# Performance work log

Measured on AMD Instinct MI355X. Metric: run time of the kernel, lower is better.

## Reference

```python
import jax, jax.numpy as jnp
import numpy as np

CL = 256   # context_length (global in original code)
IL = 64    # inst_length (global in original code)
PC, CH1, CH2, CH3 = 64, 128, 256, 256
CK1, CK2, CK3 = 3, 3, 3
CS1, CS2, CS3 = 1, 2, 2
CP1, CP2, CP3 = 1, 1, 1
BCH1, BCH2, BCH3 = 64, 128, 256
F1, OUT = 1024, 2
B = 2048
C3_OUT = 64 * CH3            # 16384, per __init__ formula with CL-1=255
F1_IN = C3_OUT + BCH3        # 16640


def _conv1d(x, W, b, stride, pad):
    # x: [B, Cin, L], W: [Cout, Cin, K]
    y = jax.lax.conv_general_dilated(x, W, window_strides=(stride,),
                                     padding=[(pad, pad)],
                                     dimension_numbers=("NCH", "OIH", "NCH"))
    return y + b[None, :, None]


def setup_inputs() -> dict:
    key = jax.random.key(0)
    ks = jax.random.split(key, 20)
    s = lambda *sh: 1.0 / np.sqrt(np.prod(sh[1:]))
    def w(k, *sh):
        return jax.random.normal(k, sh, dtype=jnp.float32) * s(*sh)
    return {
        "x": jax.random.normal(ks[0], (B, CL * IL), dtype=jnp.float32),
        "Wp": w(ks[1], PC, IL, 2), "bp": jnp.zeros((PC,), jnp.float32),
        "W1": w(ks[2], CH1, PC, CK1), "b1": jnp.zeros((CH1,), jnp.float32),
        "W2": w(ks[3], CH2, CH1, CK2), "b2": jnp.zeros((CH2,), jnp.float32),
        "W3": w(ks[4], CH3, CH2, CK3), "b3": jnp.zeros((CH3,), jnp.float32),
        "Wb1": w(ks[5], BCH1, IL), "bb1": jnp.zeros((BCH1,), jnp.float32),
        "Wb2": w(ks[6], BCH2, BCH1), "bb2": jnp.zeros((BCH2,), jnp.float32),
        "Wb3": w(ks[7], BCH3, BCH2), "bb3": jnp.zeros((BCH3,), jnp.float32),
        "Wfc1": w(ks[8], F1, F1_IN), "bfc1": jnp.zeros((F1,), jnp.float32),
        "Wfc2": w(ks[9], OUT, F1), "bfc2": jnp.zeros((OUT,), jnp.float32),
    }


def reference(x, Wp, bp, W1, b1, W2, b2, W3, b3,
              Wb1, bb1, Wb2, bb2, Wb3, bb3, Wfc1, bfc1, Wfc2, bfc2):
    xr = x.reshape(-1, CL, IL).transpose(0, 2, 1)   # [B, IL, CL]
    x0 = xr[:, :, 0]                                 # [B, IL]
    # Fused replacement for the convp loop: kernel-2 conv over (x0, x_i)
    # y[:, :, i-1] = Wp[:,:,0] @ x0 + Wp[:,:,1] @ x_i + bp
    y = (jnp.einsum("bi,pi->bp", x0, Wp[:, :, 0])[:, :, None]
         + jnp.einsum("bic,pi->bpc", xr[:, :, 1:], Wp[:, :, 1])
         + bp[None, :, None])                        # [B, PC, CL-1]
    # bypass path on the first instruction (kernel-size-1 convs == matmuls)
    f = jax.nn.relu(x0 @ Wb1.T + bb1)
    f = jax.nn.relu(f @ Wb2.T + bb2)
    f = jax.nn.relu(f @ Wb3.T + bb3)                 # [B, BCH3]
    h = jax.nn.relu(y)
    h = jax.nn.relu(_conv1d(h, W1, b1, CS1, CP1))
    h = jax.nn.relu(_conv1d(h, W2, b2, CS2, CP2))
    h = jax.nn.relu(_conv1d(h, W3, b3, CS3, CP3))    # [B, CH3, 64]
    h = h.reshape(h.shape[0], C3_OUT)
    z = jnp.concatenate([h, f], axis=1)              # [B, F1_IN]
    z = jax.nn.relu(z @ Wfc1.T + bfc1)
    return z @ Wfc2.T + bfc2                         # [B, OUT]
```

## Files before the change

### kernel.cpp

```cpp
#include <hip/hip_runtime.h>
#include <cstdint>
#include <cstddef>

typedef __attribute__((ext_vector_type(8))) short bf16x8;
typedef __attribute__((ext_vector_type(8))) unsigned short ushort8;
typedef __attribute__((ext_vector_type(4))) float f32x4;

__device__ __forceinline__ unsigned short f2bf(float f){
  unsigned int u = __float_as_uint(f);
  unsigned int lsb = (u >> 16) & 1u;
  u += 0x7fffu + lsb;
  return (unsigned short)(u >> 16);
}

__device__ __forceinline__ void gload16(const void* g, void* l){
  __builtin_amdgcn_global_load_lds(
      (const __attribute__((address_space(1))) unsigned int*)g,
      (__attribute__((address_space(3))) unsigned int*)l, 16, 0, 0);
}

__global__ __launch_bounds__(256) void pack_w_bf16_kernel(const float* __restrict__ W,
    unsigned short* __restrict__ Wb, int COUT, int CIN){
  int idx = blockIdx.x*256 + threadIdx.x;
  int tot = COUT*CIN*3;
  if (idx >= tot) return;
  int o = idx/(CIN*3); int r = idx - o*(CIN*3); int kk = r/CIN; int ci = r - kk*CIN;
  Wb[idx] = f2bf(W[(o*CIN + ci)*3 + kk]);
}

__global__ __launch_bounds__(256) void pack_wp_kernel(const float* __restrict__ Wp,
                                                      unsigned short* __restrict__ Bw){
  int idx = blockIdx.x*256 + threadIdx.x;
  if (idx >= 64*128) return;
  int p = idx >> 7, k = idx & 127;
  float v = (k < 64) ? Wp[p*128 + k*2] : Wp[p*128 + (k-64)*2 + 1];
  Bw[idx] = f2bf(v);
}

__global__ __launch_bounds__(256) void f2bf_kernel(const float* __restrict__ src,
                                                   unsigned short* __restrict__ dst, int n){
  int i = blockIdx.x*256 + threadIdx.x;
  if (i < n) dst[i] = f2bf(src[i]);
}

__global__ __launch_bounds__(256) void zero_guards_kernel(unsigned short* __restrict__ buf,
                                                          int LINP, int CIN, int nb){
  int idx = blockIdx.x*256 + threadIdx.x;
  int per = 2*CIN/8;
  if (idx >= nb*per) return;
  int b = idx / per, r = idx - b*per;
  int g = r / (CIN/8), c8 = r - g*(CIN/8);
  ushort8 z = {0,0,0,0,0,0,0,0};
  *(ushort8*)(buf + ((size_t)b*LINP + (size_t)g*(LINP-1))*CIN + c8*8) = z;
}

__global__ __launch_bounds__(256) void branch_kernel(const float* __restrict__ x,
    const float* __restrict__ Wb1, const float* __restrict__ bb1,
    const float* __restrict__ Wb2, const float* __restrict__ bb2,
    const float* __restrict__ Wb3, const float* __restrict__ bb3,
    unsigned short* __restrict__ Hcat){
  __shared__ float s0[64], s1[64], s2[128];
  const int b = blockIdx.x, tid = threadIdx.x;
  const float* xb = x + (size_t)b*16384;
  if (tid < 64) s0[tid] = xb[tid];
  __syncthreads();
  if (tid < 64){
    float a = bb1[tid];
    for (int k=0;k<64;k++) a = fmaf(Wb1[tid*64+k], s0[k], a);
    s1[tid] = fmaxf(a, 0.f);
  }
  __syncthreads();
  if (tid < 128){
    float a = bb2[tid];
    for (int k=0;k<64;k++) a = fmaf(Wb2[tid*64+k], s1[k], a);
    s2[tid] = fmaxf(a, 0.f);
  }
  __syncthreads();
  float a = bb3[tid];
  for (int k=0;k<128;k++) a = fmaf(Wb3[tid*128+k], s2[k], a);
  Hcat[(size_t)b*16640 + 16384 + tid] = f2bf(fmaxf(a, 0.f));
}

__global__ __launch_bounds__(256) void h0_gemm_kernel(const float* __restrict__ x,
    const unsigned short* __restrict__ Bw, const float* __restrict__ bp,
    unsigned short* __restrict__ h0o){
  __shared__ __align__(16) char sAraw[128*256];
  __shared__ __align__(16) char sBraw[64*256];
  const int tid = threadIdx.x;
  const int m0 = blockIdx.x*128;
  #pragma unroll
  for (int i=0;i<16;i++){
    int j = tid + 256*i;
    int row = j >> 5, q = j & 31;
    int m = m0 + row;
    int b = m / 255, c = m - b*255;
    const float* xb = x + (size_t)b*16384;
    int k = q*4;
    const float* src = (k < 64) ? (xb + k) : (xb + (c+1)*64 + (k-64));
    float4 v = *(const float4*)src;
    ushort4 u; u.x=f2bf(v.x); u.y=f2bf(v.y); u.z=f2bf(v.z); u.w=f2bf(v.w);
    *(ushort4*)(sAraw + row*256 + ((k*2) ^ ((row&7)<<4))) = u;
  }
  #pragma unroll
  for (int i=0;i<4;i++){
    int j = tid + 256*i;
    int row = j >> 4, q = j & 15;
    int k = q*8;
    ushort8 u = *(const ushort8*)(Bw + row*128 + k);
    *(ushort8*)(sBraw + row*256 + ((k*2) ^ ((row&7)<<4))) = u;
  }
  __syncthreads();
  const int lane = tid & 63, wid = tid >> 6;
  const int lr = lane & 15, lg = lane >> 4;
  f32x4 acc[2][4];
  #pragma unroll
  for (int a=0;a<2;a++)
    #pragma unroll
    for (int j=0;j<4;j++) acc[a][j] = (f32x4){0,0,0,0};
  #pragma unroll
  for (int ks=0; ks<4; ks++){
    int k = ks*32 + lg*8;
    bf16x8 af[2], bfr[4];
    #pragma unroll
    for (int f=0; f<2; f++){
      int row = wid*32 + f*16 + lr;
      af[f] = *(const bf16x8*)(sAraw + row*256 + ((k*2) ^ ((row&7)<<4)));
    }
    #pragma unroll
    for (int f=0; f<4; f++){
      int row = f*16 + lr;
      bfr[f] = *(const bf16x8*)(sBraw + row*256 + ((k*2) ^ ((row&7)<<4)));
    }
    #pragma unroll
    for (int fi=0; fi<2; fi++)
      #pragma unroll
      for (int fj=0; fj<4; fj++)
        acc[fi][fj] = __builtin_amdgcn_mfma_f32_16x16x32_bf16(af[fi], bfr[fj], acc[fi][fj], 0,0,0);
  }
  #pragma unroll
  for (int fi=0; fi<2; fi++)
    #pragma unroll
    for (int fj=0; fj<4; fj++)
      #pragma unroll
      for (int j=0;j<4;j++){
        int m = m0 + wid*32 + fi*16 + lg*4 + j;
        int n = fj*16 + lr;
        int b = m / 255, t = m - b*255;
        h0o[((size_t)b*257 + t + 1)*64 + n] = f2bf(fmaxf(acc[fi][fj][j] + bp[n], 0.f));
      }
}

template<int CIN,int COUT,int S,int LINP,int LOUT,bool TO_HCAT>
__global__ __launch_bounds__(256) void conv_gemm_kernel(
    const unsigned short* __restrict__ in, const unsigned short* __restrict__ Wb,
    const float* __restrict__ bias, unsigned short* __restrict__ out){
  constexpr int K = 3*CIN;
  constexpr int KS = K/64;
  __shared__ __align__(16) char sA[2*128*128];
  __shared__ __align__(16) char sB[2*128*128];
  const int tid = threadIdx.x;
  int m0;
  {
    int bid = blockIdx.x, nwg = gridDim.x;
    if ((nwg & 7) == 0){ int q = nwg >> 3; m0 = ((bid & 7)*q + (bid >> 3))*128; }
    else m0 = bid*128;
  }
  const int n0 = blockIdx.y*128;
  const int lane = tid & 63, wid = tid >> 6;
  const int wm = wid >> 1, wn = wid & 1;
  const int lr = lane & 15, lg = lane >> 4;
  const int srow = lane >> 3;
  const int soff = (((lane&7) ^ srow) << 3);
  const unsigned short* abase[4];
  const unsigned short* bbase[4];
  #pragma unroll
  for (int s=0;s<4;s++){
    int row = wid*32 + s*8 + srow;
    int m = m0 + row;
    int b = m / LOUT, t = m - b*LOUT;
    abase[s] = in + ((size_t)b*LINP + (size_t)t*S)*CIN + soff;
    bbase[s] = Wb + (size_t)(n0+row)*K + soff;
  }
  f32x4 acc[4][4];
  #pragma unroll
  for (int i=0;i<4;i++)
    #pragma unroll
    for (int j=0;j<4;j++) acc[i][j] = (f32x4){0,0,0,0};

  auto stage = [&](int ks, int bufi){
    const int k0 = ks*64;
    #pragma unroll
    for (int s=0;s<4;s++){
      gload16(abase[s] + k0, sA + bufi*16384 + wid*4096 + s*1024);
      gload16(bbase[s] + k0, sB + bufi*16384 + wid*4096 + s*1024);
    }
  };
  stage(0, 0);
  __syncthreads();
  int buf = 0;
  #pragma unroll
  for (int ks=0; ks<KS; ks++){
    if (ks+1 < KS) stage(ks+1, buf^1);
    #pragma unroll
    for (int kss=0; kss<2; kss++){
      const int k = kss*32 + lg*8;
      bf16x8 af[4], bfr[4];
      #pragma unroll
      for (int f=0;f<4;f++){
        int ra = wm*64 + f*16 + lr;
        af[f]  = *(const bf16x8*)(sA + buf*16384 + ra*128 + ((k*2) ^ ((ra&7)<<4)));
        int rb = wn*64 + f*16 + lr;
        bfr[f] = *(const bf16x8*)(sB + buf*16384 + rb*128 + ((k*2) ^ ((rb&7)<<4)));
      }
      #pragma unroll
      for (int fi=0;fi<4;fi++)
        #pragma unroll
        for (int fj=0;fj<4;fj++)
          acc[fi][fj] = __builtin_amdgcn_mfma_f32_16x16x32_bf16(af[fi], bfr[fj], acc[fi][fj], 0,0,0);
    }
    __syncthreads();
    buf ^= 1;
  }
  #pragma unroll
  for (int fi=0;fi<4;fi++)
    #pragma unroll
    for (int fj=0;fj<4;fj++)
      #pragma unroll
      for (int j=0;j<4;j++){
        int m = m0 + wm*64 + fi*16 + lg*4 + j;
        int n = n0 + wn*64 + fj*16 + lr;
        int b = m / LOUT, t = m - b*LOUT;
        float val = fmaxf(acc[fi][fj][j] + bias[n], 0.f);
        if (TO_HCAT) out[(size_t)b*16640 + (size_t)n*64 + t] = f2bf(val);
        else         out[((size_t)b*(LOUT+2) + t + 1)*COUT + n] = f2bf(val);
      }
}

__global__ __launch_bounds__(256) void fc1_gemm_kernel(
    const unsigned short* __restrict__ A, const unsigned short* __restrict__ Bw,
    float* __restrict__ zp, int zoffm, int MT, int KZ){
  __shared__ __align__(16) char sA[2*128*128];
  __shared__ __align__(16) char sB[2*128*128];
  const int tid = threadIdx.x;
  const int nwg = gridDim.x;
  const int lgid = (blockIdx.x % 8)*(nwg/8) + blockIdx.x/8;
  const int kz  = lgid / (8*MT);
  const int rem = lgid % (8*MT);
  const int nt  = rem / MT;
  const int mt  = rem % MT;
  const int n0 = nt*128, m0 = mt*128;
  const int lane = tid & 63, wid = tid >> 6;
  const int wm = wid >> 1, wn = wid & 1;
  const int lr = lane & 15, lg = lane >> 4;
  const int srow = lane >> 3;
  const int soff = (((lane&7) ^ srow) << 3);
  f32x4 acc[4][4];
  #pragma unroll
  for (int i=0;i<4;i++)
    #pragma unroll
    for (int j=0;j<4;j++) acc[i][j] = (f32x4){0,0,0,0};
  const int it0 = (kz*260)/KZ, it1 = ((kz+1)*260)/KZ;

  auto stage = [&](int it, int bufi){
    const size_t k0 = (size_t)it*64;
    #pragma unroll
    for (int s=0;s<4;s++){
      int row = wid*32 + s*8 + srow;
      gload16(A  + (size_t)(m0+row)*16640 + k0 + soff, sA + bufi*16384 + wid*4096 + s*1024);
      gload16(Bw + (size_t)(n0+row)*16640 + k0 + soff, sB + bufi*16384 + wid*4096 + s*1024);
    }
  };
  stage(it0, 0);
  __syncthreads();
  int buf = 0;
  for (int it=it0; it<it1; ++it){
    if (it+1 < it1) stage(it+1, buf^1);
    #pragma unroll
    for (int ks=0; ks<2; ks++){
      const int k = ks*32 + lg*8;
      bf16x8 af[4], bfr[4];
      #pragma unroll
      for (int f=0;f<4;f++){
        int rowa = wm*64 + f*16 + lr;
        af[f]  = *(const bf16x8*)(sA + buf*16384 + rowa*128 + ((k*2) ^ ((rowa&7)<<4)));
        int rowb = wn*64 + f*16 + lr;
        bfr[f] = *(const bf16x8*)(sB + buf*16384 + rowb*128 + ((k*2) ^ ((rowb&7)<<4)));
      }
      #pragma unroll
      for (int fi=0;fi<4;fi++)
        #pragma unroll
        for (int fj=0;fj<4;fj++)
          acc[fi][fj] = __builtin_amdgcn_mfma_f32_16x16x32_bf16(af[fi], bfr[fj], acc[fi][fj], 0,0,0);
    }
    __syncthreads();
    buf ^= 1;
  }
  float* zo = zp + (size_t)kz*zoffm;
  #pragma unroll
  for (int fi=0;fi<4;fi++)
    #pragma unroll
    for (int fj=0;fj<4;fj++)
      #pragma unroll
      for (int j=0;j<4;j++){
        int m = m0 + wm*64 + fi*16 + lg*4 + j;
        int n = n0 + wn*64 + fj*16 + lr;
        zo[(size_t)m*1024 + n] = acc[fi][fj][j];
      }
}

__global__ __launch_bounds__(256) void fc2_kernel(const float* __restrict__ zp, int zoffm, int KZ,
    const float* __restrict__ bfc1, const float* __restrict__ Wfc2,
    const float* __restrict__ bfc2, float* __restrict__ out){
  __shared__ float red[4][2];
  const int b = blockIdx.x, tid = threadIdx.x;
  float a0 = 0.f, a1 = 0.f;
  for (int n = tid; n < 1024; n += 256){
    float s = bfc1[n];
    const float* zb = zp + (size_t)b*1024 + n;
    for (int kz = 0; kz < KZ; kz++) s += zb[(size_t)kz*zoffm];
    s = fmaxf(s, 0.f);
    a0 = fmaf(s, Wfc2[n], a0);
    a1 = fmaf(s, Wfc2[1024+n], a1);
  }
  #pragma unroll
  for (int m=32; m>=1; m>>=1){ a0 += __shfl_xor(a0, m, 64); a1 += __shfl_xor(a1, m, 64); }
  const int w = tid >> 6;
  if ((tid & 63) == 0){ red[w][0] = a0; red[w][1] = a1; }
  __syncthreads();
  if (tid == 0){
    out[(size_t)b*2]   = red[0][0]+red[1][0]+red[2][0]+red[3][0] + bfc2[0];
    out[(size_t)b*2+1] = red[0][1]+red[1][1]+red[2][1]+red[3][1] + bfc2[1];
  }
}

extern "C" void kernel_launch(void* const* d_in, const int* in_sizes, int n_in,
                              void* d_out, int out_size, void* d_ws, size_t ws_size,
                              hipStream_t stream){
  const float* x    = (const float*)d_in[0];
  const float* Wp   = (const float*)d_in[1];
  const float* bp   = (const float*)d_in[2];
  const float* W1   = (const float*)d_in[3];
  const float* b1   = (const float*)d_in[4];
  const float* W2   = (const float*)d_in[5];
  const float* b2   = (const float*)d_in[6];
  const float* W3   = (const float*)d_in[7];
  const float* b3   = (const float*)d_in[8];
  const float* Wb1  = (const float*)d_in[9];
  const float* bb1  = (const float*)d_in[10];
  const float* Wb2  = (const float*)d_in[11];
  const float* bb2  = (const float*)d_in[12];
  const float* Wb3  = (const float*)d_in[13];
  const float* bb3  = (const float*)d_in[14];
  const float* Wfc1 = (const float*)d_in[15];
  const float* bfc1 = (const float*)d_in[16];
  const float* Wfc2 = (const float*)d_in[17];
  const float* bfc2 = (const float*)d_in[18];
  float* out = (float*)d_out;

  size_t off = 0;
  char* basep = (char*)d_ws;
  auto carve = [&](size_t bytes)->char*{
    char* q = basep + off; off += (bytes + 255) & ~(size_t)255; return q;
  };
  unsigned short* W1b   = (unsigned short*)carve((size_t)128*3*64*2);
  unsigned short* W2b   = (unsigned short*)carve((size_t)256*3*128*2);
  unsigned short* W3b   = (unsigned short*)carve((size_t)256*3*256*2);
  unsigned short* Bwp   = (unsigned short*)carve((size_t)64*128*2);
  unsigned short* Wfc1b = (unsigned short*)carve((size_t)1024*16640*2);
  size_t fixed = off;

  int Bc = 128, KZ = 64;
  {
    const int bcs[5] = {2048, 1024, 512, 256, 128};
    const int kzs[5] = {4, 8, 16, 32, 64};
    for (int i = 0; i < 5; i++){
      size_t b = bcs[i];
      size_t need = fixed + b*((size_t)66560+65792+33280) + (size_t)kzs[i]*b*4096 + 16*256;
      if (need <= ws_size){ Bc = bcs[i]; KZ = kzs[i]; break; }
    }
  }
  const int NC = 2048/Bc;
  const int MT = Bc/128;
  unsigned short* buf1 = (unsigned short*)carve((size_t)Bc*66560);
  unsigned short* buf2 = (unsigned short*)carve((size_t)Bc*65792);
  unsigned short* Hcat = (unsigned short*)carve((size_t)Bc*33280);
  float*          zp   = (float*)carve((size_t)KZ*Bc*4096);
  const int zoffm = Bc*1024;

  hipLaunchKernelGGL(pack_w_bf16_kernel, dim3((128*64*3+255)/256), dim3(256), 0, stream, W1, W1b, 128, 64);
  hipLaunchKernelGGL(pack_w_bf16_kernel, dim3((256*128*3+255)/256), dim3(256), 0, stream, W2, W2b, 256, 128);
  hipLaunchKernelGGL(pack_w_bf16_kernel, dim3((256*256*3+255)/256), dim3(256), 0, stream, W3, W3b, 256, 256);
  hipLaunchKernelGGL(pack_wp_kernel, dim3(32), dim3(256), 0, stream, Wp, Bwp);
  hipLaunchKernelGGL(f2bf_kernel, dim3((17039360+255)/256), dim3(256), 0, stream, Wfc1, Wfc1b, 17039360);

  for (int c = 0; c < NC; ++c){
    const float* xc = x + (size_t)c*Bc*16384;
    hipLaunchKernelGGL(zero_guards_kernel, dim3((Bc*2*64/8+255)/256), dim3(256), 0, stream,
                       buf1, 257, 64, Bc);
    hipLaunchKernelGGL(zero_guards_kernel, dim3((Bc*2*128/8+255)/256), dim3(256), 0, stream,
                       buf2, 257, 128, Bc);
    hipLaunchKernelGGL(branch_kernel, dim3(Bc), dim3(256), 0, stream,
                       xc, Wb1, bb1, Wb2, bb2, Wb3, bb3, Hcat);
    hipLaunchKernelGGL(h0_gemm_kernel, dim3(Bc*255/128), dim3(256), 0, stream, xc, Bwp, bp, buf1);
    hipLaunchKernelGGL((conv_gemm_kernel<64,128,1,257,255,false>), dim3(Bc*255/128, 1), dim3(256), 0, stream,
                       buf1, W1b, b1, buf2);
    hipLaunchKernelGGL(zero_guards_kernel, dim3((Bc*2*256/8+255)/256), dim3(256), 0, stream,
                       buf1, 130, 256, Bc);
    hipLaunchKernelGGL((conv_gemm_kernel<128,256,2,257,128,false>), dim3(Bc, 2), dim3(256), 0, stream,
                       buf2, W2b, b2, buf1);
    hipLaunchKernelGGL((conv_gemm_kernel<256,256,2,130,64,true>), dim3(Bc/2, 2), dim3(256), 0, stream,
                       buf1, W3b, b3, Hcat);
    hipLaunchKernelGGL(fc1_gemm_kernel, dim3(8*MT*KZ), dim3(256), 0, stream,
                       Hcat, Wfc1b, zp, zoffm, MT, KZ);
    hipLaunchKernelGGL(fc2_kernel, dim3(Bc), dim3(256), 0, stream,
                       zp, zoffm, KZ, bfc1, Wfc2, bfc2, out + (size_t)c*Bc*2);
  }
}
```

Before: 547.5 us.

## Replace im2col conv GEMM with per-batch input window staged once in LDS

```diff
diff --git a/kernel.cpp b/kernel.cpp
--- a/kernel.cpp
+++ b/kernel.cpp
@@ -150,70 +150,82 @@
       }
 }
 
-template<int CIN,int COUT,int S,int LINP,int LOUT,bool TO_HCAT>
-__global__ __launch_bounds__(256) void conv_gemm_kernel(
+template<int CIN,int COUT,int S,int LOUT,int PADIN,int PADOUT,int BM,bool TO_HCAT>
+__global__ __launch_bounds__(256) void conv_win_kernel(
     const unsigned short* __restrict__ in, const unsigned short* __restrict__ Wb,
     const float* __restrict__ bias, unsigned short* __restrict__ out){
-  constexpr int K = 3*CIN;
-  constexpr int KS = K/64;
-  __shared__ __align__(16) char sA[2*128*128];
-  __shared__ __align__(16) char sB[2*128*128];
-  const int tid = threadIdx.x;
-  int m0;
-  {
-    int bid = blockIdx.x, nwg = gridDim.x;
-    if ((nwg & 7) == 0){ int q = nwg >> 3; m0 = ((bid & 7)*q + (bid >> 3))*128; }
-    else m0 = bid*128;
-  }
-  const int n0 = blockIdx.y*128;
-  const int lane = tid & 63, wid = tid >> 6;
+  constexpr int K3  = 3*CIN, NCH = K3/64;
+  constexpr int MPB = (LOUT + BM - 1)/BM;
+  constexpr int NT  = COUT/128;
+  constexpr int MF  = BM/32;
+  constexpr int WR  = (BM-1)*S + 3;
+  constexpr int CP8 = CIN/8;
+  constexpr int CB  = CIN*2;
+  constexpr int NSLOT = WR*CP8;
+  __shared__ __align__(16) char SA[WR*CB];
+  __shared__ __align__(16) char SB[2*16384];
+  const int tid = threadIdx.x, lane = tid & 63, wid = tid >> 6;
+  int lgid;
+  { int bid = blockIdx.x, nwg = gridDim.x;
+    lgid = ((nwg & 7)==0) ? ((bid & 7)*(nwg>>3) + (bid>>3)) : bid; }
+  const int nt = lgid % NT;
+  const int tile = lgid / NT;
+  const int b = tile / MPB, mt = tile % MPB;
+  const int t0 = mt*BM, n0 = nt*128;
+  const unsigned short* Abase = in + ((size_t)b*PADIN + (size_t)t0*S)*CIN;
+  const int rowlim = PADIN - t0*S;
+
+  for (int i=0; i*256 < NSLOT; ++i){
+    int slot = i*256 + tid;
+    if (slot < NSLOT){
+      int row = slot/CP8, p = slot - row*CP8;
+      if (row < rowlim)
+        gload16(Abase + (size_t)row*CIN + ((p ^ ((row>>(S-1))&7))<<3), SA + slot*16);
+      else
+        *(ushort8*)(SA + slot*16) = (ushort8){0,0,0,0,0,0,0,0};
+    }
+  }
+  const int srow = lane >> 3;
+  const int bsoff = (((lane&7) ^ srow) << 3);
+  auto stageB = [&](int c, int bufi){
+    #pragma unroll
+    for (int s=0;s<4;s++){
+      int row = wid*32 + s*8 + srow;
+      gload16(Wb + (size_t)(n0+row)*K3 + c*64 + bsoff, SB + bufi*16384 + wid*4096 + s*1024);
+    }
+  };
+  stageB(0, 0);
+  __syncthreads();
+
   const int wm = wid >> 1, wn = wid & 1;
   const int lr = lane & 15, lg = lane >> 4;
-  const int srow = lane >> 3;
-  const int soff = (((lane&7) ^ srow) << 3);
-  const unsigned short* abase[4];
-  const unsigned short* bbase[4];
-  #pragma unroll
-  for (int s=0;s<4;s++){
-    int row = wid*32 + s*8 + srow;
-    int m = m0 + row;
-    int b = m / LOUT, t = m - b*LOUT;
-    abase[s] = in + ((size_t)b*LINP + (size_t)t*S)*CIN + soff;
-    bbase[s] = Wb + (size_t)(n0+row)*K + soff;
-  }
-  f32x4 acc[4][4];
-  #pragma unroll
-  for (int i=0;i<4;i++)
+  f32x4 acc[MF][4];
+  #pragma unroll
+  for (int i=0;i<MF;i++)
     #pragma unroll
     for (int j=0;j<4;j++) acc[i][j] = (f32x4){0,0,0,0};
 
-  auto stage = [&](int ks, int bufi){
-    const int k0 = ks*64;
-    #pragma unroll
-    for (int s=0;s<4;s++){
-      gload16(abase[s] + k0, sA + bufi*16384 + wid*4096 + s*1024);
-      gload16(bbase[s] + k0, sB + bufi*16384 + wid*4096 + s*1024);
-    }
-  };
-  stage(0, 0);
-  __syncthreads();
   int buf = 0;
   #pragma unroll
-  for (int ks=0; ks<KS; ks++){
-    if (ks+1 < KS) stage(ks+1, buf^1);
-    #pragma unroll
-    for (int kss=0; kss<2; kss++){
-      const int k = kss*32 + lg*8;
-      bf16x8 af[4], bfr[4];
+  for (int c=0;c<NCH;c++){
+    if (c+1 < NCH) stageB(c+1, buf^1);
+    const int kk = c/(CIN/64), cc = c - kk*(CIN/64);
+    #pragma unroll
+    for (int ks=0; ks<2; ks++){
+      bf16x8 af[MF], bfr[4];
+      #pragma unroll
+      for (int f=0;f<MF;f++){
+        int row = (wm*(MF*16) + f*16 + lr)*S + kk;
+        int ci = cc*8 + ks*4 + lg;
+        af[f] = *(const bf16x8*)(SA + (size_t)row*CB + ((ci ^ ((row>>(S-1))&7))<<4));
+      }
       #pragma unroll
       for (int f=0;f<4;f++){
-        int ra = wm*64 + f*16 + lr;
-        af[f]  = *(const bf16x8*)(sA + buf*16384 + ra*128 + ((k*2) ^ ((ra&7)<<4)));
         int rb = wn*64 + f*16 + lr;
-        bfr[f] = *(const bf16x8*)(sB + buf*16384 + rb*128 + ((k*2) ^ ((rb&7)<<4)));
-      }
-      #pragma unroll
-      for (int fi=0;fi<4;fi++)
+        bfr[f] = *(const bf16x8*)(SB + buf*16384 + rb*128 + (((ks*4+lg) ^ (rb&7))<<4));
+      }
+      #pragma unroll
+      for (int fi=0;fi<MF;fi++)
         #pragma unroll
         for (int fj=0;fj<4;fj++)
           acc[fi][fj] = __builtin_amdgcn_mfma_f32_16x16x32_bf16(af[fi], bfr[fj], acc[fi][fj], 0,0,0);
@@ -221,18 +233,20 @@
     __syncthreads();
     buf ^= 1;
   }
-  #pragma unroll
-  for (int fi=0;fi<4;fi++)
+
+  #pragma unroll
+  for (int fi=0;fi<MF;fi++)
     #pragma unroll
     for (int fj=0;fj<4;fj++)
       #pragma unroll
       for (int j=0;j<4;j++){
-        int m = m0 + wm*64 + fi*16 + lg*4 + j;
+        int t = t0 + wm*(MF*16) + fi*16 + lg*4 + j;
         int n = n0 + wn*64 + fj*16 + lr;
-        int b = m / LOUT, t = m - b*LOUT;
-        float val = fmaxf(acc[fi][fj][j] + bias[n], 0.f);
-        if (TO_HCAT) out[(size_t)b*16640 + (size_t)n*64 + t] = f2bf(val);
-        else         out[((size_t)b*(LOUT+2) + t + 1)*COUT + n] = f2bf(val);
+        if (MPB*BM == LOUT || t < LOUT){
+          float v = fmaxf(acc[fi][fj][j] + bias[n], 0.f);
+          if (TO_HCAT) out[(size_t)b*16640 + (size_t)n*64 + t] = f2bf(v);
+          else         out[((size_t)b*PADOUT + t + 1)*COUT + n] = f2bf(v);
+        }
       }
 }
 
@@ -402,14 +416,14 @@
     hipLaunchKernelGGL(branch_kernel, dim3(Bc), dim3(256), 0, stream,
                        xc, Wb1, bb1, Wb2, bb2, Wb3, bb3, Hcat);
     hipLaunchKernelGGL(h0_gemm_kernel, dim3(Bc*255/128), dim3(256), 0, stream, xc, Bwp, bp, buf1);
-    hipLaunchKernelGGL((conv_gemm_kernel<64,128,1,257,255,false>), dim3(Bc*255/128, 1), dim3(256), 0, stream,
-                       buf1, W1b, b1, buf2);
+    hipLaunchKernelGGL((conv_win_kernel<64,128,1,255,257,257,128,false>),
+                       dim3(Bc*2), dim3(256), 0, stream, buf1, W1b, b1, buf2);
     hipLaunchKernelGGL(zero_guards_kernel, dim3((Bc*2*256/8+255)/256), dim3(256), 0, stream,
                        buf1, 130, 256, Bc);
-    hipLaunchKernelGGL((conv_gemm_kernel<128,256,2,257,128,false>), dim3(Bc, 2), dim3(256), 0, stream,
-                       buf2, W2b, b2, buf1);
-    hipLaunchKernelGGL((conv_gemm_kernel<256,256,2,130,64,true>), dim3(Bc/2, 2), dim3(256), 0, stream,
-                       buf1, W3b, b3, Hcat);
+    hipLaunchKernelGGL((conv_win_kernel<128,256,2,128,257,130,64,false>),
+                       dim3(Bc*4), dim3(256), 0, stream, buf2, W2b, b2, buf1);
+    hipLaunchKernelGGL((conv_win_kernel<256,256,2,64,130,0,32,true>),
+                       dim3(Bc*4), dim3(256), 0, stream, buf1, W3b, b3, Hcat);
     hipLaunchKernelGGL(fc1_gemm_kernel, dim3(8*MT*KZ), dim3(256), 0, stream,
                        Hcat, Wfc1b, zp, zoffm, MT, KZ);
     hipLaunchKernelGGL(fc2_kernel, dim3(Bc), dim3(256), 0, stream,
```

Result: slower. 579.4 us (+5.8%).

## Use 256x128 single-buffered tiles with 512 threads in conv GEMMs

Applied to the files above, without the earlier changes.

```diff
diff --git a/kernel.cpp b/kernel.cpp
--- a/kernel.cpp
+++ b/kernel.cpp
@@ -151,19 +151,19 @@
 }
 
 template<int CIN,int COUT,int S,int LINP,int LOUT,bool TO_HCAT>
-__global__ __launch_bounds__(256) void conv_gemm_kernel(
+__global__ __launch_bounds__(512) void conv_gemm_kernel(
     const unsigned short* __restrict__ in, const unsigned short* __restrict__ Wb,
-    const float* __restrict__ bias, unsigned short* __restrict__ out){
+    const float* __restrict__ bias, unsigned short* __restrict__ out, int M){
   constexpr int K = 3*CIN;
   constexpr int KS = K/64;
-  __shared__ __align__(16) char sA[2*128*128];
-  __shared__ __align__(16) char sB[2*128*128];
+  __shared__ __align__(16) char sA[256*128];
+  __shared__ __align__(16) char sB[128*128];
   const int tid = threadIdx.x;
   int m0;
   {
     int bid = blockIdx.x, nwg = gridDim.x;
-    if ((nwg & 7) == 0){ int q = nwg >> 3; m0 = ((bid & 7)*q + (bid >> 3))*128; }
-    else m0 = bid*128;
+    if ((nwg & 7) == 0){ int q = nwg >> 3; m0 = ((bid & 7)*q + (bid >> 3))*256; }
+    else m0 = bid*256;
   }
   const int n0 = blockIdx.y*128;
   const int lane = tid & 63, wid = tid >> 6;
@@ -172,13 +172,17 @@
   const int srow = lane >> 3;
   const int soff = (((lane&7) ^ srow) << 3);
   const unsigned short* abase[4];
-  const unsigned short* bbase[4];
+  const unsigned short* bbase[2];
   #pragma unroll
   for (int s=0;s<4;s++){
-    int row = wid*32 + s*8 + srow;
-    int m = m0 + row;
+    int m = m0 + wid*32 + s*8 + srow;
+    if (m >= M) m = M-1;
     int b = m / LOUT, t = m - b*LOUT;
     abase[s] = in + ((size_t)b*LINP + (size_t)t*S)*CIN + soff;
+  }
+  #pragma unroll
+  for (int s=0;s<2;s++){
+    int row = wid*16 + s*8 + srow;
     bbase[s] = Wb + (size_t)(n0+row)*K + soff;
   }
   f32x4 acc[4][4];
@@ -187,20 +191,15 @@
     #pragma unroll
     for (int j=0;j<4;j++) acc[i][j] = (f32x4){0,0,0,0};
 
-  auto stage = [&](int ks, int bufi){
+  #pragma unroll
+  for (int ks=0; ks<KS; ks++){
     const int k0 = ks*64;
-    #pragma unroll
-    for (int s=0;s<4;s++){
-      gload16(abase[s] + k0, sA + bufi*16384 + wid*4096 + s*1024);
-      gload16(bbase[s] + k0, sB + bufi*16384 + wid*4096 + s*1024);
-    }
-  };
-  stage(0, 0);
-  __syncthreads();
-  int buf = 0;
-  #pragma unroll
-  for (int ks=0; ks<KS; ks++){
-    if (ks+1 < KS) stage(ks+1, buf^1);
+    __syncthreads();
+    #pragma unroll
+    for (int s=0;s<4;s++) gload16(abase[s] + k0, sA + wid*4096 + s*1024);
+    #pragma unroll
+    for (int s=0;s<2;s++) gload16(bbase[s] + k0, sB + wid*2048 + s*1024);
+    __syncthreads();
     #pragma unroll
     for (int kss=0; kss<2; kss++){
       const int k = kss*32 + lg*8;
@@ -208,9 +207,9 @@
       #pragma unroll
       for (int f=0;f<4;f++){
         int ra = wm*64 + f*16 + lr;
-        af[f]  = *(const bf16x8*)(sA + buf*16384 + ra*128 + ((k*2) ^ ((ra&7)<<4)));
+        af[f]  = *(const bf16x8*)(sA + ra*128 + ((k*2) ^ ((ra&7)<<4)));
         int rb = wn*64 + f*16 + lr;
-        bfr[f] = *(const bf16x8*)(sB + buf*16384 + rb*128 + ((k*2) ^ ((rb&7)<<4)));
+        bfr[f] = *(const bf16x8*)(sB + rb*128 + ((k*2) ^ ((rb&7)<<4)));
       }
       #pragma unroll
       for (int fi=0;fi<4;fi++)
@@ -218,8 +217,6 @@
         for (int fj=0;fj<4;fj++)
           acc[fi][fj] = __builtin_amdgcn_mfma_f32_16x16x32_bf16(af[fi], bfr[fj], acc[fi][fj], 0,0,0);
     }
-    __syncthreads();
-    buf ^= 1;
   }
   #pragma unroll
   for (int fi=0;fi<4;fi++)
@@ -229,10 +226,12 @@
       for (int j=0;j<4;j++){
         int m = m0 + wm*64 + fi*16 + lg*4 + j;
         int n = n0 + wn*64 + fj*16 + lr;
-        int b = m / LOUT, t = m - b*LOUT;
-        float val = fmaxf(acc[fi][fj][j] + bias[n], 0.f);
-        if (TO_HCAT) out[(size_t)b*16640 + (size_t)n*64 + t] = f2bf(val);
-        else         out[((size_t)b*(LOUT+2) + t + 1)*COUT + n] = f2bf(val);
+        if (m < M){
+          int b = m / LOUT, t = m - b*LOUT;
+          float val = fmaxf(acc[fi][fj][j] + bias[n], 0.f);
+          if (TO_HCAT) out[(size_t)b*16640 + (size_t)n*64 + t] = f2bf(val);
+          else         out[((size_t)b*(LOUT+2) + t + 1)*COUT + n] = f2bf(val);
+        }
       }
 }
 
@@ -402,14 +401,23 @@
     hipLaunchKernelGGL(branch_kernel, dim3(Bc), dim3(256), 0, stream,
                        xc, Wb1, bb1, Wb2, bb2, Wb3, bb3, Hcat);
     hipLaunchKernelGGL(h0_gemm_kernel, dim3(Bc*255/128), dim3(256), 0, stream, xc, Bwp, bp, buf1);
-    hipLaunchKernelGGL((conv_gemm_kernel<64,128,1,257,255,false>), dim3(Bc*255/128, 1), dim3(256), 0, stream,
-                       buf1, W1b, b1, buf2);
+    {
+      int M = Bc*255, gx = (M + 255)/256;
+      hipLaunchKernelGGL((conv_gemm_kernel<64,128,1,257,255,false>), dim3(gx, 1), dim3(512), 0, stream,
+                         buf1, W1b, b1, buf2, M);
+    }
     hipLaunchKernelGGL(zero_guards_kernel, dim3((Bc*2*256/8+255)/256), dim3(256), 0, stream,
                        buf1, 130, 256, Bc);
-    hipLaunchKernelGGL((conv_gemm_kernel<128,256,2,257,128,false>), dim3(Bc, 2), dim3(256), 0, stream,
-                       buf2, W2b, b2, buf1);
-    hipLaunchKernelGGL((conv_gemm_kernel<256,256,2,130,64,true>), dim3(Bc/2, 2), dim3(256), 0, stream,
-                       buf1, W3b, b3, Hcat);
+    {
+      int M = Bc*128;
+      hipLaunchKernelGGL((conv_gemm_kernel<128,256,2,257,128,false>), dim3(M/256, 2), dim3(512), 0, stream,
+                         buf2, W2b, b2, buf1, M);
+    }
+    {
+      int M = Bc*64;
+      hipLaunchKernelGGL((conv_gemm_kernel<256,256,2,130,64,true>), dim3(M/256, 2), dim3(512), 0, stream,
+                         buf1, W3b, b3, Hcat, M);
+    }
     hipLaunchKernelGGL(fc1_gemm_kernel, dim3(8*MT*KZ), dim3(256), 0, stream,
                        Hcat, Wfc1b, zp, zoffm, MT, KZ);
     hipLaunchKernelGGL(fc2_kernel, dim3(Bc), dim3(256), 0, stream,
```

Result: slower. 563.2 us (+2.9%).

## Fuse input projection and first conv into one per-sample kernel

Applied to the files above, without the earlier changes.

```diff
diff --git a/kernel.cpp b/kernel.cpp
--- a/kernel.cpp
+++ b/kernel.cpp
@@ -11,6 +11,11 @@
   unsigned int lsb = (u >> 16) & 1u;
   u += 0x7fffu + lsb;
   return (unsigned short)(u >> 16);
+}
+
+__device__ __forceinline__ ushort8 cvt8(const float4 a, const float4 b){
+  ushort8 u; u[0]=f2bf(a.x); u[1]=f2bf(a.y); u[2]=f2bf(a.z); u[3]=f2bf(a.w);
+  u[4]=f2bf(b.x); u[5]=f2bf(b.y); u[6]=f2bf(b.z); u[7]=f2bf(b.w); return u;
 }
 
 __device__ __forceinline__ void gload16(const void* g, void* l){
@@ -28,13 +33,12 @@
   Wb[idx] = f2bf(W[(o*CIN + ci)*3 + kk]);
 }
 
-__global__ __launch_bounds__(256) void pack_wp_kernel(const float* __restrict__ Wp,
-                                                      unsigned short* __restrict__ Bw){
+__global__ __launch_bounds__(256) void pack_bh_kernel(const float* __restrict__ Wp,
+                                                      unsigned short* __restrict__ Bh){
   int idx = blockIdx.x*256 + threadIdx.x;
-  if (idx >= 64*128) return;
-  int p = idx >> 7, k = idx & 127;
-  float v = (k < 64) ? Wp[p*128 + k*2] : Wp[p*128 + (k-64)*2 + 1];
-  Bw[idx] = f2bf(v);
+  if (idx >= 64*64) return;
+  int p = idx >> 6, i = idx & 63;
+  Bh[idx] = f2bf(Wp[p*128 + i*2 + 1]);
 }
 
 __global__ __launch_bounds__(256) void f2bf_kernel(const float* __restrict__ src,
@@ -81,73 +85,132 @@
   Hcat[(size_t)b*16640 + 16384 + tid] = f2bf(fmaxf(a, 0.f));
 }
 
-__global__ __launch_bounds__(256) void h0_gemm_kernel(const float* __restrict__ x,
-    const unsigned short* __restrict__ Bw, const float* __restrict__ bp,
-    unsigned short* __restrict__ h0o){
-  __shared__ __align__(16) char sAraw[128*256];
-  __shared__ __align__(16) char sBraw[64*256];
-  const int tid = threadIdx.x;
-  const int m0 = blockIdx.x*128;
-  #pragma unroll
-  for (int i=0;i<16;i++){
-    int j = tid + 256*i;
-    int row = j >> 5, q = j & 31;
-    int m = m0 + row;
-    int b = m / 255, c = m - b*255;
-    const float* xb = x + (size_t)b*16384;
-    int k = q*4;
-    const float* src = (k < 64) ? (xb + k) : (xb + (c+1)*64 + (k-64));
-    float4 v = *(const float4*)src;
-    ushort4 u; u.x=f2bf(v.x); u.y=f2bf(v.y); u.z=f2bf(v.z); u.w=f2bf(v.w);
-    *(ushort4*)(sAraw + row*256 + ((k*2) ^ ((row&7)<<4))) = u;
-  }
+__global__ __launch_bounds__(512) void fused1_kernel(
+    const float* __restrict__ x, const float* __restrict__ Wp, const float* __restrict__ bp,
+    const unsigned short* __restrict__ Bh, const unsigned short* __restrict__ W1b,
+    const float* __restrict__ b1, unsigned short* __restrict__ c1p){
+  __shared__ __align__(16) char S[115392];
+  constexpr int SX = 0;
+  constexpr int SH = 37008;
+  constexpr int SB = 74160;
+  constexpr int SW = 106928;
+  constexpr int SY = 115120;
+  const int b = blockIdx.x, tid = threadIdx.x;
+  const int lane = tid & 63, wv = tid >> 6;
+  const int lr = lane & 15, lg = lane >> 4;
+  const float* xg = x + (size_t)b*16384;
+
   #pragma unroll
   for (int i=0;i<4;i++){
-    int j = tid + 256*i;
-    int row = j >> 4, q = j & 15;
-    int k = q*8;
-    ushort8 u = *(const ushort8*)(Bw + row*128 + k);
-    *(ushort8*)(sBraw + row*256 + ((k*2) ^ ((row&7)<<4))) = u;
-  }
-  __syncthreads();
-  const int lane = tid & 63, wid = tid >> 6;
-  const int lr = lane & 15, lg = lane >> 4;
-  f32x4 acc[2][4];
-  #pragma unroll
-  for (int a=0;a<2;a++)
-    #pragma unroll
-    for (int j=0;j<4;j++) acc[a][j] = (f32x4){0,0,0,0};
-  #pragma unroll
-  for (int ks=0; ks<4; ks++){
-    int k = ks*32 + lg*8;
-    bf16x8 af[2], bfr[4];
-    #pragma unroll
-    for (int f=0; f<2; f++){
-      int row = wid*32 + f*16 + lr;
-      af[f] = *(const bf16x8*)(sAraw + row*256 + ((k*2) ^ ((row&7)<<4)));
-    }
-    #pragma unroll
-    for (int f=0; f<4; f++){
-      int row = f*16 + lr;
-      bfr[f] = *(const bf16x8*)(sBraw + row*256 + ((k*2) ^ ((row&7)<<4)));
-    }
-    #pragma unroll
-    for (int fi=0; fi<2; fi++)
-      #pragma unroll
-      for (int fj=0; fj<4; fj++)
-        acc[fi][fj] = __builtin_amdgcn_mfma_f32_16x16x32_bf16(af[fi], bfr[fj], acc[fi][fj], 0,0,0);
-  }
-  #pragma unroll
-  for (int fi=0; fi<2; fi++)
-    #pragma unroll
-    for (int fj=0; fj<4; fj++)
-      #pragma unroll
-      for (int j=0;j<4;j++){
-        int m = m0 + wid*32 + fi*16 + lg*4 + j;
-        int n = fj*16 + lr;
-        int b = m / 255, t = m - b*255;
-        h0o[((size_t)b*257 + t + 1)*64 + n] = f2bf(fmaxf(acc[fi][fj][j] + bp[n], 0.f));
-      }
+    int s = tid + 512*i;
+    int row = s>>3, sl = s&7;
+    const float4* src = (const float4*)(xg + row*64 + sl*8);
+    *(ushort8*)(S + SX + row*144 + sl*16) = cvt8(src[0], src[1]);
+  }
+  { int row = tid>>3, sl = tid&7;
+    ushort8 u = *(const ushort8*)(Bh + row*64 + sl*8);
+    *(ushort8*)(S + SW + row*128 + ((sl*16)^((row&7)<<4))) = u; }
+  ushort8 z8 = {0,0,0,0,0,0,0,0};
+  if (tid < 9)        *(ushort8*)(S + SX + 256*144 + tid*16) = z8;
+  else if (tid < 18)  *(ushort8*)(S + SH + 0*144   + (tid-9)*16) = z8;
+  else if (tid < 27)  *(ushort8*)(S + SH + 257*144 + (tid-18)*16) = z8;
+  if (tid < 64){
+    float a = bp[tid];
+    const float* wr = Wp + tid*128;
+    #pragma unroll 8
+    for (int i=0;i<64;i++) a = fmaf(wr[2*i], xg[i], a);
+    *(float*)(S + SY + tid*4) = a;
+  }
+  __syncthreads();
+
+  {
+    const int wm = wv>>1, wn = wv&1;
+    f32x4 acc[4][2];
+    #pragma unroll
+    for (int i=0;i<4;i++){ acc[i][0]=(f32x4){0,0,0,0}; acc[i][1]=(f32x4){0,0,0,0}; }
+    #pragma unroll
+    for (int ks=0; ks<2; ks++){
+      int k = ks*32 + lg*8;
+      bf16x8 af[4], bf[2];
+      #pragma unroll
+      for (int f=0;f<4;f++){ int ar = wm*64 + f*16 + lr + 1;
+        af[f] = *(const bf16x8*)(S + SX + ar*144 + k*2); }
+      #pragma unroll
+      for (int f=0;f<2;f++){ int rb = wn*32 + f*16 + lr;
+        bf[f] = *(const bf16x8*)(S + SW + rb*128 + ((k*2)^((rb&7)<<4))); }
+      #pragma unroll
+      for (int i=0;i<4;i++)
+        #pragma unroll
+        for (int j=0;j<2;j++)
+          acc[i][j] = __builtin_amdgcn_mfma_f32_16x16x32_bf16(af[i], bf[j], acc[i][j], 0,0,0);
+    }
+    #pragma unroll
+    for (int fm=0;fm<4;fm++)
+      #pragma unroll
+      for (int fn=0;fn<2;fn++)
+        #pragma unroll
+        for (int j=0;j<4;j++){
+          int t = wm*64 + fm*16 + lg*4 + j;
+          int p = wn*32 + fn*16 + lr;
+          float v = acc[fm][fn][j] + *(const float*)(S + SY + p*4);
+          unsigned short o = (t < 255) ? f2bf(fmaxf(v, 0.f)) : (unsigned short)0;
+          *(unsigned short*)(S + SH + (t+1)*144 + p*2) = o;
+        }
+  }
+
+  {
+    const int soff = ((lane&7)^(lane>>3))<<3;
+    const int rbase = wv*8 + (lane>>3);
+    #pragma unroll
+    for (int s=0;s<2;s++)
+      gload16(W1b + (size_t)(s*64 + rbase)*192 + soff, S + SB + s*8192 + wv*1024);
+    __syncthreads();
+
+    const int wm = wv>>1, wn = wv&1;
+    f32x4 acc[4][4];
+    #pragma unroll
+    for (int i=0;i<4;i++)
+      #pragma unroll
+      for (int j=0;j<4;j++) acc[i][j] = (f32x4){0,0,0,0};
+    #pragma unroll
+    for (int c=0;c<3;c++){
+      int buf = c&1;
+      if (c<2){
+        #pragma unroll
+        for (int s=0;s<2;s++)
+          gload16(W1b + (size_t)(s*64 + rbase)*192 + (c+1)*64 + soff,
+                  S + SB + (buf^1)*16384 + s*8192 + wv*1024);
+      }
+      #pragma unroll
+      for (int ks=0; ks<2; ks++){
+        int k = ks*32 + lg*8;
+        bf16x8 af[4], bf[4];
+        #pragma unroll
+        for (int f=0;f<4;f++){ int ar = wm*64 + f*16 + lr + c;
+          af[f] = *(const bf16x8*)(S + SH + ar*144 + k*2); }
+        #pragma unroll
+        for (int f=0;f<4;f++){ int rb = wn*64 + f*16 + lr;
+          bf[f] = *(const bf16x8*)(S + SB + buf*16384 + rb*128 + ((k*2)^((rb&7)<<4))); }
+        #pragma unroll
+        for (int i=0;i<4;i++)
+          #pragma unroll
+          for (int j=0;j<4;j++)
+            acc[i][j] = __builtin_amdgcn_mfma_f32_16x16x32_bf16(af[i], bf[j], acc[i][j], 0,0,0);
+      }
+      __syncthreads();
+    }
+    unsigned short* cbo = c1p + (size_t)b*32896;
+    #pragma unroll
+    for (int fi=0;fi<4;fi++)
+      #pragma unroll
+      for (int fj=0;fj<4;fj++)
+        #pragma unroll
+        for (int j=0;j<4;j++){
+          int t = wm*64 + fi*16 + lg*4 + j;
+          int n = wn*64 + fj*16 + lr;
+          if (t < 255) cbo[(size_t)(t+1)*128 + n] = f2bf(fmaxf(acc[fi][fj][j] + b1[n], 0.f));
+        }
+  }
 }
 
 template<int CIN,int COUT,int S,int LINP,int LOUT,bool TO_HCAT>
@@ -365,7 +428,7 @@
   unsigned short* W1b   = (unsigned short*)carve((size_t)128*3*64*2);
   unsigned short* W2b   = (unsigned short*)carve((size_t)256*3*128*2);
   unsigned short* W3b   = (unsigned short*)carve((size_t)256*3*256*2);
-  unsigned short* Bwp   = (unsigned short*)carve((size_t)64*128*2);
+  unsigned short* Bhp   = (unsigned short*)carve((size_t)64*64*2);
   unsigned short* Wfc1b = (unsigned short*)carve((size_t)1024*16640*2);
   size_t fixed = off;
 
@@ -390,22 +453,19 @@
   hipLaunchKernelGGL(pack_w_bf16_kernel, dim3((128*64*3+255)/256), dim3(256), 0, stream, W1, W1b, 128, 64);
   hipLaunchKernelGGL(pack_w_bf16_kernel, dim3((256*128*3+255)/256), dim3(256), 0, stream, W2, W2b, 256, 128);
   hipLaunchKernelGGL(pack_w_bf16_kernel, dim3((256*256*3+255)/256), dim3(256), 0, stream, W3, W3b, 256, 256);
-  hipLaunchKernelGGL(pack_wp_kernel, dim3(32), dim3(256), 0, stream, Wp, Bwp);
+  hipLaunchKernelGGL(pack_bh_kernel, dim3(16), dim3(256), 0, stream, Wp, Bhp);
   hipLaunchKernelGGL(f2bf_kernel, dim3((17039360+255)/256), dim3(256), 0, stream, Wfc1, Wfc1b, 17039360);
 
   for (int c = 0; c < NC; ++c){
     const float* xc = x + (size_t)c*Bc*16384;
-    hipLaunchKernelGGL(zero_guards_kernel, dim3((Bc*2*64/8+255)/256), dim3(256), 0, stream,
-                       buf1, 257, 64, Bc);
     hipLaunchKernelGGL(zero_guards_kernel, dim3((Bc*2*128/8+255)/256), dim3(256), 0, stream,
                        buf2, 257, 128, Bc);
+    hipLaunchKernelGGL(zero_guards_kernel, dim3((Bc*2*256/8+255)/256), dim3(256), 0, stream,
+                       buf1, 130, 256, Bc);
     hipLaunchKernelGGL(branch_kernel, dim3(Bc), dim3(256), 0, stream,
                        xc, Wb1, bb1, Wb2, bb2, Wb3, bb3, Hcat);
-    hipLaunchKernelGGL(h0_gemm_kernel, dim3(Bc*255/128), dim3(256), 0, stream, xc, Bwp, bp, buf1);
-    hipLaunchKernelGGL((conv_gemm_kernel<64,128,1,257,255,false>), dim3(Bc*255/128, 1), dim3(256), 0, stream,
-                       buf1, W1b, b1, buf2);
-    hipLaunchKernelGGL(zero_guards_kernel, dim3((Bc*2*256/8+255)/256), dim3(256), 0, stream,
-                       buf1, 130, 256, Bc);
+    hipLaunchKernelGGL(fused1_kernel, dim3(Bc), dim3(512), 0, stream,
+                       xc, Wp, bp, Bhp, W1b, b1, buf2);
     hipLaunchKernelGGL((conv_gemm_kernel<128,256,2,257,128,false>), dim3(Bc, 2), dim3(256), 0, stream,
                        buf2, W2b, b2, buf1);
     hipLaunchKernelGGL((conv_gemm_kernel<256,256,2,130,64,true>), dim3(Bc/2, 2), dim3(256), 0, stream,
```

After: 575.9 us. 1.05x slower.
